# Optimization experiments

Hardware: AMD Instinct MI355X
Metric: run time of the kernel (lower is better)

## Reference

```python
import jax, jax.numpy as jnp
import numpy as np

B, T, D = 4, 2048, 1024
H, HD = 16, 64  # num_heads, head_size; H*HD == D
DFF = 4 * D
EPS = 1e-5

def _ln(x, g, b):
    mu = jnp.mean(x, axis=-1, keepdims=True)
    var = jnp.mean(jnp.square(x - mu), axis=-1, keepdims=True)
    return (x - mu) * jax.lax.rsqrt(var + EPS) * g + b

def setup_inputs() -> dict:
    key = jax.random.key(0)
    ks = jax.random.split(key, 12)
    s = lambda fan_in: 1.0 / np.sqrt(fan_in)
    return {
        "x": jax.random.normal(ks[0], (B, T, D), jnp.float32),
        "Wq": jax.random.normal(ks[1], (H, D, HD), jnp.float32) * s(D),
        "Wk": jax.random.normal(ks[2], (H, D, HD), jnp.float32) * s(D),
        "Wv": jax.random.normal(ks[3], (H, D, HD), jnp.float32) * s(D),
        "Wo": jax.random.normal(ks[4], (D, D), jnp.float32) * s(D),
        "bo": jax.random.normal(ks[5], (D,), jnp.float32) * 0.01,
        "W1": jax.random.normal(ks[6], (D, DFF), jnp.float32) * s(D),
        "b1": jax.random.normal(ks[7], (DFF,), jnp.float32) * 0.01,
        "W2": jax.random.normal(ks[8], (DFF, D), jnp.float32) * s(DFF),
        "b2": jax.random.normal(ks[9], (D,), jnp.float32) * 0.01,
        "g1": jnp.ones((D,), jnp.float32),
        "be1": jnp.zeros((D,), jnp.float32),
        "g2": jnp.ones((D,), jnp.float32),
        "be2": jnp.zeros((D,), jnp.float32),
    }

def reference(x, Wq, Wk, Wv, Wo, bo, W1, b1, W2, b2, g1, be1, g2, be2):
    # pre-LN attention
    h = _ln(x, g1, be1)                                   # [B,T,D]
    q = jnp.einsum('btd,hde->bhte', h, Wq)                # [B,H,T,HD]
    k = jnp.einsum('btd,hde->bhte', h, Wk)
    v = jnp.einsum('btd,hde->bhte', h, Wv)
    scores = jnp.einsum('bhte,bhse->bhts', q, k) * (HD ** -0.5)  # [B,H,T,T]
    mask = jnp.tril(jnp.ones((T, T), bool))
    scores = jnp.where(mask, scores, -jnp.inf)
    attn = jax.nn.softmax(scores, axis=-1)
    ctx = jnp.einsum('bhts,bhse->bhte', attn, v)          # [B,H,T,HD]
    ctx = ctx.transpose(0, 2, 1, 3).reshape(B, T, D)      # concat heads
    x = x + jnp.einsum('btd,de->bte', ctx, Wo) + bo
    # pre-LN FFN
    h2 = _ln(x, g2, be2)
    ff = jax.nn.relu(jnp.einsum('btd,df->btf', h2, W1) + b1)
    x = x + jnp.einsum('btf,fd->btd', ff, W2) + b2
    return x
```

## Files before the change

kernel.cpp:

```cpp
#include <hip/hip_runtime.h>
#include <stdint.h>

#define B_ 4
#define T_ 2048
#define D_ 1024
#define H_ 16
#define HD_ 64
#define DFF_ 4096
#define M_ (B_ * T_)

typedef __bf16 bf16x8 __attribute__((ext_vector_type(8)));
typedef float f32x4 __attribute__((ext_vector_type(4)));

__device__ __forceinline__ uint16_t f2bf(float f) {
  union { float f; uint32_t u; } v;
  v.f = f;
  uint32_t r = v.u + 0x7FFF + ((v.u >> 16) & 1);
  return (uint16_t)(r >> 16);
}

#define GLD_LDS(gp, lp)                                                        \
  __builtin_amdgcn_global_load_lds(                                            \
      (const __attribute__((address_space(1))) void*)(gp),                     \
      (__attribute__((address_space(3))) void*)(lp), 16, 0, 0)

__global__ __launch_bounds__(256) void ln_bf16(const float* __restrict__ x,
                                               const float* __restrict__ gamma,
                                               const float* __restrict__ beta,
                                               uint16_t* __restrict__ out) {
  __shared__ float red[4];
  const int tid = threadIdx.x;
  const size_t row = blockIdx.x;
  const float4 v = ((const float4*)(x + row * D_))[tid];
  float s = v.x + v.y + v.z + v.w;
#pragma unroll
  for (int off = 32; off >= 1; off >>= 1) s += __shfl_xor(s, off, 64);
  if ((tid & 63) == 0) red[tid >> 6] = s;
  __syncthreads();
  const float mean = (red[0] + red[1] + red[2] + red[3]) * (1.0f / D_);
  const float d0 = v.x - mean, d1 = v.y - mean, d2 = v.z - mean, d3 = v.w - mean;
  float ss = d0 * d0 + d1 * d1 + d2 * d2 + d3 * d3;
#pragma unroll
  for (int off = 32; off >= 1; off >>= 1) ss += __shfl_xor(ss, off, 64);
  __syncthreads();
  if ((tid & 63) == 0) red[tid >> 6] = ss;
  __syncthreads();
  const float var = (red[0] + red[1] + red[2] + red[3]) * (1.0f / D_);
  const float rstd = rsqrtf(var + 1e-5f);
  const float4 g = ((const float4*)gamma)[tid];
  const float4 b = ((const float4*)beta)[tid];
  ushort4 o;
  o.x = f2bf(d0 * rstd * g.x + b.x);
  o.y = f2bf(d1 * rstd * g.y + b.y);
  o.z = f2bf(d2 * rstd * g.z + b.z);
  o.w = f2bf(d3 * rstd * g.w + b.w);
  ((ushort4*)(out + row * D_))[tid] = o;
}

__global__ __launch_bounds__(256) void prep_ln(
    const float* __restrict__ x, const float* __restrict__ g1,
    const float* __restrict__ be1, uint16_t* __restrict__ hbuf,
    const float* __restrict__ Wq, const float* __restrict__ Wk,
    const float* __restrict__ Wv, const float* __restrict__ Wo,
    const float* __restrict__ W1, const float* __restrict__ W2,
    uint16_t* __restrict__ wqkvt, uint16_t* __restrict__ wot,
    uint16_t* __restrict__ w1t, uint16_t* __restrict__ w2t) {
  const int pid = blockIdx.x;
  const int tid = threadIdx.x;

  if (pid < 8192) {
    __shared__ float red[4];
    const size_t row = pid;
    const float4 v = ((const float4*)(x + row * D_))[tid];
    float s = v.x + v.y + v.z + v.w;
#pragma unroll
    for (int off = 32; off >= 1; off >>= 1) s += __shfl_xor(s, off, 64);
    if ((tid & 63) == 0) red[tid >> 6] = s;
    __syncthreads();
    const float mean = (red[0] + red[1] + red[2] + red[3]) * (1.0f / D_);
    const float d0 = v.x - mean, d1 = v.y - mean, d2 = v.z - mean, d3 = v.w - mean;
    float ss = d0 * d0 + d1 * d1 + d2 * d2 + d3 * d3;
#pragma unroll
    for (int off = 32; off >= 1; off >>= 1) ss += __shfl_xor(ss, off, 64);
    __syncthreads();
    if ((tid & 63) == 0) red[tid >> 6] = ss;
    __syncthreads();
    const float var = (red[0] + red[1] + red[2] + red[3]) * (1.0f / D_);
    const float rstd = rsqrtf(var + 1e-5f);
    const float4 g = ((const float4*)g1)[tid];
    const float4 b = ((const float4*)be1)[tid];
    ushort4 o;
    o.x = f2bf(d0 * rstd * g.x + b.x);
    o.y = f2bf(d1 * rstd * g.y + b.y);
    o.z = f2bf(d2 * rstd * g.z + b.z);
    o.w = f2bf(d3 * rstd * g.w + b.w);
    ((ushort4*)(hbuf + row * D_))[tid] = o;
    return;
  }

  __shared__ float tile[32][33];
  const int tx = tid & 31, ty = tid >> 5;
  const int q = pid - 8192;

  if (q >= 9216) {
    const int p = q - 9216;
    const int bx = p & 1, by = (p >> 1) & 31, z = p >> 6;
    const int which = z >> 4, hh = z & 15;
    const float* W = (which == 0) ? Wq : ((which == 1) ? Wk : Wv);
    const float* in = W + (size_t)hh * D_ * HD_;
    const int e0 = bx * 32, d0 = by * 32;
#pragma unroll
    for (int i = 0; i < 32; i += 8)
      tile[ty + i][tx] = in[(size_t)(d0 + ty + i) * HD_ + e0 + tx];
    __syncthreads();
#pragma unroll
    for (int i = 0; i < 32; i += 8)
      wqkvt[((size_t)(which * 1024 + hh * 64) + e0 + ty + i) * D_ + d0 + tx] =
          f2bf(tile[tx][ty + i]);
    return;
  }

  const float* in;
  uint16_t* out;
  int R, C, bx, by;
  if (q < 1024) {
    in = Wo; out = wot; R = 1024; C = 1024; bx = q & 31; by = q >> 5;
  } else if (q < 5120) {
    const int p = q - 1024;
    in = W1; out = w1t; R = 1024; C = 4096; bx = p & 127; by = p >> 7;
  } else {
    const int p = q - 5120;
    in = W2; out = w2t; R = 4096; C = 1024; bx = p & 31; by = p >> 5;
  }
  const int c0 = bx * 32, r0 = by * 32;
#pragma unroll
  for (int i = 0; i < 32; i += 8)
    tile[ty + i][tx] = in[(size_t)(r0 + ty + i) * C + c0 + tx];
  __syncthreads();
#pragma unroll
  for (int i = 0; i < 32; i += 8)
    out[(size_t)(c0 + ty + i) * R + r0 + tx] = f2bf(tile[tx][ty + i]);
}

template <int BN>
__global__ __launch_bounds__(256) void gemm_bf16(const uint16_t* __restrict__ A,
                                                 const uint16_t* __restrict__ Bt,
                                                 void* __restrict__ C,
                                                 const float* __restrict__ bias,
                                                 const float* __restrict__ resid,
                                                 int M, int N, int K, int lda,
                                                 int ldb, int flags) {
  constexpr int NJ = BN / 32;
  __shared__ __align__(16) uint16_t As[128 * 64];
  __shared__ __align__(16) uint16_t Bs[BN * 64];
  const int tid = threadIdx.x;
  const int lane = tid & 63, w = tid >> 6;
  const int quad = lane >> 4, lr = lane & 15;
  const int wr = w >> 1, wc = w & 1;

  const int n_tiles = N / BN;
  const int pid = blockIdx.x;
  const int grp = 16 * n_tiles;
  const int gid = pid / grp;
  const int rem = pid - gid * grp;
  const int nt = rem / 16;
  const int mt = gid * 16 + (rem - nt * 16);
  const int bn0 = nt * BN, bm0 = mt * 128;

  f32x4 acc[4][NJ];
#pragma unroll
  for (int i = 0; i < 4; i++)
#pragma unroll
    for (int j = 0; j < NJ; j++) acc[i][j] = f32x4{0.f, 0.f, 0.f, 0.f};

  const int s_row = lane >> 3, s_slot = lane & 7;

  for (int k0 = 0; k0 < K; k0 += 64) {
#pragma unroll
    for (int u = 0; u < 4; u++) {
      const int r = w * 32 + u * 8 + s_row;
      const int cg = s_slot ^ (r & 7);
      GLD_LDS(A + (size_t)(bm0 + r) * lda + k0 + cg * 8, As + (w * 32 + u * 8) * 64);
    }
#pragma unroll
    for (int u = 0; u < NJ; u++) {
      const int r = w * (BN / 4) + u * 8 + s_row;
      const int cg = s_slot ^ (r & 7);
      GLD_LDS(Bt + (size_t)(bn0 + r) * ldb + k0 + cg * 8,
              Bs + (w * (BN / 4) + u * 8) * 64);
    }
    __syncthreads();

#pragma unroll
    for (int ks = 0; ks < 2; ks++) {
      bf16x8 af[4], bfr[NJ];
#pragma unroll
      for (int i = 0; i < 4; i++) {
        const int m = wr * 64 + i * 16 + lr;
        const int slot = (ks * 4 + quad) ^ (m & 7);
        af[i] = *(const bf16x8*)(As + m * 64 + slot * 8);
      }
#pragma unroll
      for (int j = 0; j < NJ; j++) {
        const int n = wc * (BN / 2) + j * 16 + lr;
        const int slot = (ks * 4 + quad) ^ (n & 7);
        bfr[j] = *(const bf16x8*)(Bs + n * 64 + slot * 8);
      }
#pragma unroll
      for (int i = 0; i < 4; i++)
#pragma unroll
        for (int j = 0; j < NJ; j++)
          acc[i][j] =
              __builtin_amdgcn_mfma_f32_16x16x32_bf16(af[i], bfr[j], acc[i][j], 0, 0, 0);
    }
    __syncthreads();
  }

  const int base_m = bm0 + wr * 64 + quad * 4;
  const int base_n = bn0 + wc * (BN / 2) + lr;
#pragma unroll
  for (int i = 0; i < 4; i++) {
#pragma unroll
    for (int j = 0; j < NJ; j++) {
      const int col = base_n + j * 16;
      const float bv = bias ? bias[col] : 0.f;
#pragma unroll
      for (int r = 0; r < 4; r++) {
        const size_t row = base_m + i * 16 + r;
        float v = acc[i][j][r] + bv;
        if (resid) v += resid[row * N + col];
        if (flags & 1) v = fmaxf(v, 0.f);
        if (flags & 2)
          ((uint16_t*)C)[row * N + col] = f2bf(v);
        else
          ((float*)C)[row * N + col] = v;
      }
    }
  }
}

#define STAGE8(buf, kt)                                                        \
  do {                                                                         \
    const int k0s = (kt) * 64;                                                 \
    _Pragma("unroll") for (int u = 0; u < 4; u++) {                            \
      const int r = w * 32 + u * 8 + s_row;                                    \
      const int cg = s_slot ^ (r & 7);                                         \
      GLD_LDS(A + (size_t)(bm0 + r) * lda + k0s + cg * 8,                      \
              &As[buf][(w * 32 + u * 8) * 64]);                                \
      GLD_LDS(Bt + (size_t)(bn0 + r) * ldb + k0s + cg * 8,                     \
              &Bs[buf][(w * 32 + u * 8) * 64]);                                \
    }                                                                          \
  } while (0)

#define RD_A8(dst, ibase, ks)                                                  \
  _Pragma("unroll") for (int i = 0; i < 4; i++) {                              \
    const int m = wr * 128 + ((ibase) + i) * 16 + lr;                          \
    const int slot = ((ks) * 4 + quad) ^ (m & 7);                              \
    dst[i] = *(const bf16x8*)(&As[c][m * 64 + slot * 8]);                      \
  }

#define RD_B8(dst, ks)                                                         \
  _Pragma("unroll") for (int j = 0; j < 4; j++) {                              \
    const int n = wc * 64 + j * 16 + lr;                                       \
    const int slot = ((ks) * 4 + quad) ^ (n & 7);                              \
    dst[j] = *(const bf16x8*)(&Bs[c][n * 64 + slot * 8]);                      \
  }

#define MFMA16(ibase, aarr)                                                    \
  do {                                                                         \
    __builtin_amdgcn_s_setprio(1);                                             \
    _Pragma("unroll") for (int i = 0; i < 4; i++)                              \
        _Pragma("unroll") for (int j = 0; j < 4; j++) acc[(ibase) + i][j] =    \
        __builtin_amdgcn_mfma_f32_16x16x32_bf16(aarr[i], bb[j],                \
                                                acc[(ibase) + i][j], 0, 0, 0); \
    __builtin_amdgcn_s_setprio(0);                                             \
  } while (0)

__global__ __launch_bounds__(512, 2) void gemm_8ph(
    const uint16_t* __restrict__ A, const uint16_t* __restrict__ Bt,
    void* __restrict__ C, const float* __restrict__ bias,
    const float* __restrict__ resid, int M, int N, int K, int lda, int ldb,
    int flags) {
  __shared__ __align__(16) uint16_t As[2][256 * 64];
  __shared__ __align__(16) uint16_t Bs[2][256 * 64];
  const int tid = threadIdx.x;
  const int lane = tid & 63, w = tid >> 6;
  const int quad = lane >> 4, lr = lane & 15;
  const int wr = w >> 2, wc = w & 3;
  const int s_row = lane >> 3, s_slot = lane & 7;

  const int nwg = gridDim.x;
  const int cpx = nwg >> 3;
  const int pid0 = blockIdx.x;
  const int pid = (pid0 & 7) * cpx + (pid0 >> 3);
  const int n_tiles = N >> 8;
  const int mt = pid / n_tiles;
  const int nt = pid - mt * n_tiles;
  const int bm0 = mt * 256, bn0 = nt * 256;

  f32x4 acc[8][4];
#pragma unroll
  for (int i = 0; i < 8; i++)
#pragma unroll
    for (int j = 0; j < 4; j++) acc[i][j] = f32x4{0.f, 0.f, 0.f, 0.f};

  STAGE8(0, 0);
  asm volatile("s_waitcnt vmcnt(0)" ::: "memory");
  __builtin_amdgcn_s_barrier();

  const int NT = K >> 6;
  for (int t = 0; t < NT; ++t) {
    const int c = t & 1;
    bf16x8 a_lo[4], a_hi[4], bb[4];
    RD_A8(a_lo, 0, 0);
    RD_B8(bb, 0);
    if (t + 1 < NT) STAGE8(c ^ 1, t + 1);
    __builtin_amdgcn_s_barrier();
    MFMA16(0, a_lo);
    __builtin_amdgcn_s_barrier();
    RD_A8(a_hi, 4, 0);
    __builtin_amdgcn_s_barrier();
    MFMA16(4, a_hi);
    __builtin_amdgcn_s_barrier();
    RD_A8(a_lo, 0, 1);
    RD_B8(bb, 1);
    __builtin_amdgcn_s_barrier();
    MFMA16(0, a_lo);
    __builtin_amdgcn_s_barrier();
    RD_A8(a_hi, 4, 1);
    __builtin_amdgcn_s_barrier();
    MFMA16(4, a_hi);
    asm volatile("s_waitcnt vmcnt(0)" ::: "memory");
    __builtin_amdgcn_s_barrier();
  }

  const int base_m = bm0 + wr * 128 + quad * 4;
  const int base_n = bn0 + wc * 64 + lr;
#pragma unroll
  for (int i = 0; i < 8; i++) {
#pragma unroll
    for (int j = 0; j < 4; j++) {
      const int col = base_n + j * 16;
      const float bv = bias ? bias[col] : 0.f;
#pragma unroll
      for (int r = 0; r < 4; r++) {
        const size_t row = base_m + i * 16 + r;
        float v = acc[i][j][r] + bv;
        if (resid) v += resid[row * N + col];
        if (flags & 1) v = fmaxf(v, 0.f);
        if (flags & 2)
          ((uint16_t*)C)[row * N + col] = f2bf(v);
        else
          ((float*)C)[row * N + col] = v;
      }
    }
  }
}

__global__ __launch_bounds__(256) void v_transpose(const uint16_t* __restrict__ qkv,
                                                   uint16_t* __restrict__ vtb) {
  __shared__ __align__(16) uint16_t tile[64 * 72];
  const int tid = threadIdx.x;
  const int t0 = blockIdx.x * 64;
  const int bh = blockIdx.y;
  const int b = bh >> 4, h = bh & 15;
  const uint16_t* src = qkv + (size_t)b * T_ * 3072 + 2048 + h * 64;
#pragma unroll
  for (int u = 0; u < 2; u++) {
    const int uu = tid + u * 256;
    const int r = uu >> 3, c = uu & 7;
    *(int4*)(tile + r * 72 + c * 8) =
        *(const int4*)(src + (size_t)(t0 + r) * 3072 + c * 8);
  }
  __syncthreads();
  uint16_t* dst = vtb + ((size_t)bh * 64) * T_ + t0;
#pragma unroll
  for (int u = 0; u < 2; u++) {
    const int uu = tid + u * 256;
    const int e = uu >> 3, c2 = uu & 7;
    union { uint16_t u16[8]; int4 v; } tmp;
#pragma unroll
    for (int jj = 0; jj < 8; jj++) tmp.u16[jj] = tile[(c2 * 8 + jj) * 72 + e];
    *(int4*)(dst + (size_t)e * T_ + c2 * 8) = tmp.v;
  }
}

__device__ __forceinline__ void attn_tile_compute(
    const uint16_t* __restrict__ Kb, const uint16_t* __restrict__ Vb,
    uint16_t* __restrict__ Ps, const bf16x8 (&aq)[2][2], f32x4 (&oacc)[2][4],
    float (&l_part)[2], int st, int q0, int w, int quad, int lr) {
  const int lr7 = lr & 7;
  const int row_min_w = q0 + w * 32;

  f32x4 sa[2][4];
#pragma unroll
  for (int i = 0; i < 2; i++)
#pragma unroll
    for (int sf = 0; sf < 4; sf++) sa[i][sf] = f32x4{0.f, 0.f, 0.f, 0.f};
#pragma unroll
  for (int ks = 0; ks < 2; ks++) {
    bf16x8 ak[4];
#pragma unroll
    for (int sf = 0; sf < 4; sf++) {
      const int slot = (ks * 4 + quad) ^ lr7;
      ak[sf] = *(const bf16x8*)(Kb + (sf * 16 + lr) * 64 + slot * 8);
    }
#pragma unroll
    for (int i = 0; i < 2; i++)
#pragma unroll
      for (int sf = 0; sf < 4; sf++)
        sa[i][sf] =
            __builtin_amdgcn_mfma_f32_16x16x32_bf16(ak[sf], aq[i][ks], sa[i][sf], 0, 0, 0);
  }

  const bool diag = (st * 64 + 63 > row_min_w);
  if (diag) {
#pragma unroll
    for (int i = 0; i < 2; i++) {
      const int mrow = q0 + w * 32 + i * 16 + lr;
#pragma unroll
      for (int sf = 0; sf < 4; sf++) {
        const int s0 = st * 64 + sf * 16 + quad * 4;
        float p[4];
#pragma unroll
        for (int r = 0; r < 4; r++) {
          float sv = sa[i][sf][r];
          if (s0 + r > mrow) sv = -1e30f;
          p[r] = exp2f(fmaf(sv, 0.18033688f, -28.8539008f));
          l_part[i] += p[r];
        }
        ushort4 pk;
        pk.x = f2bf(p[0]);
        pk.y = f2bf(p[1]);
        pk.z = f2bf(p[2]);
        pk.w = f2bf(p[3]);
        *(ushort4*)(Ps + (size_t)(w * 32 + i * 16 + lr) * 72 + sf * 16 + quad * 4) = pk;
      }
    }
  } else {
#pragma unroll
    for (int i = 0; i < 2; i++) {
#pragma unroll
      for (int sf = 0; sf < 4; sf++) {
        float p[4];
#pragma unroll
        for (int r = 0; r < 4; r++) {
          p[r] = exp2f(fmaf(sa[i][sf][r], 0.18033688f, -28.8539008f));
          l_part[i] += p[r];
        }
        ushort4 pk;
        pk.x = f2bf(p[0]);
        pk.y = f2bf(p[1]);
        pk.z = f2bf(p[2]);
        pk.w = f2bf(p[3]);
        *(ushort4*)(Ps + (size_t)(w * 32 + i * 16 + lr) * 72 + sf * 16 + quad * 4) = pk;
      }
    }
  }

#pragma unroll
  for (int ks = 0; ks < 2; ks++) {
    bf16x8 ap[2], bv[4];
#pragma unroll
    for (int i = 0; i < 2; i++)
      ap[i] = *(const bf16x8*)(Ps + (size_t)(w * 32 + i * 16 + lr) * 72 + ks * 32 +
                               quad * 8);
#pragma unroll
    for (int j = 0; j < 4; j++) {
      const int slot = (ks * 4 + quad) ^ lr7;
      bv[j] = *(const bf16x8*)(Vb + (j * 16 + lr) * 64 + slot * 8);
    }
#pragma unroll
    for (int i = 0; i < 2; i++)
#pragma unroll
      for (int j = 0; j < 4; j++)
        oacc[i][j] =
            __builtin_amdgcn_mfma_f32_16x16x32_bf16(ap[i], bv[j], oacc[i][j], 0, 0, 0);
  }
}

__global__ __launch_bounds__(256) void attn_mfma(const uint16_t* __restrict__ qkv,
                                                 const uint16_t* __restrict__ vtb,
                                                 uint16_t* __restrict__ ctx) {
  __shared__ __align__(16) uint16_t Ks[64 * 64];
  __shared__ __align__(16) uint16_t Vt[64 * 64];
  __shared__ __align__(16) uint16_t Ps[128 * 72];
  const int tid = threadIdx.x;
  const int lane = tid & 63, w = tid >> 6;
  const int quad = lane >> 4, lr = lane & 15;
  const int pid = blockIdx.x;
  const int bh = pid & 63;
  const int i_pair = pid >> 6;
  const int b = bh >> 4, h = bh & 15;
  const uint16_t* base = qkv + (size_t)b * T_ * 3072 + h * 64;
  const uint16_t* vbase = vtb + ((size_t)bh * 64) * T_;
  const int s_row = lane >> 3, s_slot = lane & 7;

  const int tqA = i_pair, tqB = 15 - i_pair;
  const int q0A = tqA * 128, q0B = tqB * 128;
  const int nstgA = 2 * tqA + 2, nstgB = 2 * tqB + 2;
  const int nstg = (nstgA > nstgB) ? nstgA : nstgB;

  bf16x8 aqA[2][2], aqB[2][2];
#pragma unroll
  for (int i = 0; i < 2; i++)
#pragma unroll
    for (int ks = 0; ks < 2; ks++) {
      aqA[i][ks] = *(const bf16x8*)(base + (size_t)(q0A + w * 32 + i * 16 + lr) * 3072 +
                                    ks * 32 + quad * 8);
      aqB[i][ks] = *(const bf16x8*)(base + (size_t)(q0B + w * 32 + i * 16 + lr) * 3072 +
                                    ks * 32 + quad * 8);
    }

  f32x4 oaccA[2][4], oaccB[2][4];
#pragma unroll
  for (int i = 0; i < 2; i++)
#pragma unroll
    for (int j = 0; j < 4; j++) {
      oaccA[i][j] = f32x4{0.f, 0.f, 0.f, 0.f};
      oaccB[i][j] = f32x4{0.f, 0.f, 0.f, 0.f};
    }
  float lA[2] = {0.f, 0.f}, lB[2] = {0.f, 0.f};

  const int row_maxA = q0A + w * 32 + 31;
  const int row_maxB = q0B + w * 32 + 31;

  for (int st = 0; st < nstg; st++) {
    __syncthreads();
#pragma unroll
    for (int u = 0; u < 2; u++) {
      const int r = w * 16 + u * 8 + s_row;
      const int cg = s_slot ^ (r & 7);
      GLD_LDS(base + 1024 + (size_t)(st * 64 + r) * 3072 + cg * 8,
              Ks + (w * 16 + u * 8) * 64);
      GLD_LDS(vbase + (size_t)r * T_ + st * 64 + cg * 8, Vt + (w * 16 + u * 8) * 64);
    }
    __syncthreads();

    if (st < nstgA && st * 64 <= row_maxA)
      attn_tile_compute(Ks, Vt, Ps, aqA, oaccA, lA, st, q0A, w, quad, lr);
    if (st < nstgB && st * 64 <= row_maxB)
      attn_tile_compute(Ks, Vt, Ps, aqB, oaccB, lB, st, q0B, w, quad, lr);
  }

#pragma unroll
  for (int half = 0; half < 2; half++) {
    const int q0 = half ? q0B : q0A;
    f32x4(&oacc)[2][4] = half ? oaccB : oaccA;
    float* l_part = half ? lB : lA;
    float linv[2];
#pragma unroll
    for (int i = 0; i < 2; i++) {
      float l = l_part[i];
      l += __shfl_xor(l, 16, 64);
      l += __shfl_xor(l, 32, 64);
      linv[i] = 1.f / l;
    }
    uint16_t* ob =
        ctx + ((size_t)b * T_ + q0 + w * 32 + quad * 4) * D_ + h * 64 + lr;
#pragma unroll
    for (int i = 0; i < 2; i++)
#pragma unroll
      for (int r = 0; r < 4; r++) {
        const float inv = __shfl(linv[i], quad * 4 + r, 64);
#pragma unroll
        for (int j = 0; j < 4; j++)
          ob[(size_t)(i * 16 + r) * D_ + j * 16] = f2bf(oacc[i][j][r] * inv);
      }
  }
}

extern "C" void kernel_launch(void* const* d_in, const int* in_sizes, int n_in,
                              void* d_out, int out_size, void* d_ws, size_t ws_size,
                              hipStream_t stream) {
  const float* x = (const float*)d_in[0];
  const float* Wq = (const float*)d_in[1];
  const float* Wk = (const float*)d_in[2];
  const float* Wv = (const float*)d_in[3];
  const float* Wo = (const float*)d_in[4];
  const float* bo = (const float*)d_in[5];
  const float* W1 = (const float*)d_in[6];
  const float* b1 = (const float*)d_in[7];
  const float* W2 = (const float*)d_in[8];
  const float* b2 = (const float*)d_in[9];
  const float* g1 = (const float*)d_in[10];
  const float* be1 = (const float*)d_in[11];
  const float* g2 = (const float*)d_in[12];
  const float* be2 = (const float*)d_in[13];
  float* out = (float*)d_out;

  const size_t MB = 1024ull * 1024ull;
  if (ws_size < 200 * MB) return;
  char* ws = (char*)d_ws;
  uint16_t* hbuf = (uint16_t*)(ws + 0 * MB);
  uint16_t* wqkvt = (uint16_t*)(ws + 16 * MB);
  uint16_t* wot = (uint16_t*)(ws + 22 * MB);
  uint16_t* w1t = (uint16_t*)(ws + 24 * MB);
  uint16_t* w2t = (uint16_t*)(ws + 32 * MB);
  float* x1 = (float*)(ws + 40 * MB);
  uint16_t* qkvb = (uint16_t*)(ws + 72 * MB);
  uint16_t* ctxb = (uint16_t*)(ws + 120 * MB);
  uint16_t* vtb = (uint16_t*)(ws + 136 * MB);
  uint16_t* ffb = (uint16_t*)(ws + 136 * MB);

  prep_ln<<<20480, 256, 0, stream>>>(x, g1, be1, hbuf, Wq, Wk, Wv, Wo, W1, W2,
                                     wqkvt, wot, w1t, w2t);
  gemm_8ph<<<(M_ / 256) * (3 * D_ / 256), 512, 0, stream>>>(
      hbuf, wqkvt, qkvb, nullptr, nullptr, M_, 3 * D_, D_, D_, D_, 2);
  v_transpose<<<dim3(T_ / 64, B_ * H_), 256, 0, stream>>>(qkvb, vtb);
  attn_mfma<<<512, 256, 0, stream>>>(qkvb, vtb, ctxb);
  gemm_bf16<64><<<64 * 16, 256, 0, stream>>>(ctxb, wot, x1, bo, x, M_, D_, D_, D_,
                                             D_, 0);
  ln_bf16<<<M_, 256, 0, stream>>>(x1, g2, be2, hbuf);
  gemm_8ph<<<(M_ / 256) * (DFF_ / 256), 512, 0, stream>>>(
      hbuf, w1t, ffb, b1, nullptr, M_, DFF_, D_, D_, D_, 1 | 2);
  gemm_bf16<64><<<64 * 16, 256, 0, stream>>>(ffb, w2t, out, b2, x1, M_, D_, DFF_,
                                             DFF_, DFF_, 0);
}
```

Baseline: 559.9 us.

## Split A-tile staging by half and use partial vmcnt waits in GEMM pipeline

Reorders the global-to-LDS staging so each wave loads A rows grouped by the upper and lower 128-row halves. Partial s_waitcnt vmcnt counts then let the first half of A be consumed before the second half of the prefetch has landed. The last K iteration is peeled so the steady-state loop always prefetches, and the peeled tail drops its intra-iteration barriers. The aim is to overlap the prefetch with MFMA work instead of draining all loads at the end of each iteration. The risk is that the vmcnt counts depend on exact load issue order, so any mismatch would mean reading stale LDS data.

```diff
diff --git a/kernel.cpp b/kernel.cpp
--- a/kernel.cpp
+++ b/kernel.cpp
@@ -245,10 +245,21 @@
     _Pragma("unroll") for (int u = 0; u < 4; u++) {                            \
       const int r = w * 32 + u * 8 + s_row;                                    \
       const int cg = s_slot ^ (r & 7);                                         \
-      GLD_LDS(A + (size_t)(bm0 + r) * lda + k0s + cg * 8,                      \
-              &As[buf][(w * 32 + u * 8) * 64]);                                \
       GLD_LDS(Bt + (size_t)(bn0 + r) * ldb + k0s + cg * 8,                     \
               &Bs[buf][(w * 32 + u * 8) * 64]);                                \
+    }                                                                          \
+    const int rb = (w >> 2) * 128 + (w & 3) * 16;                              \
+    _Pragma("unroll") for (int u = 0; u < 2; u++) {                            \
+      const int r = rb + u * 8 + s_row;                                        \
+      const int cg = s_slot ^ (r & 7);                                         \
+      GLD_LDS(A + (size_t)(bm0 + r) * lda + k0s + cg * 8,                      \
+              &As[buf][(rb + u * 8) * 64]);                                    \
+    }                                                                          \
+    _Pragma("unroll") for (int u = 0; u < 2; u++) {                            \
+      const int r = rb + 64 + u * 8 + s_row;                                   \
+      const int cg = s_slot ^ (r & 7);                                         \
+      GLD_LDS(A + (size_t)(bm0 + r) * lda + k0s + cg * 8,                      \
+              &As[buf][(rb + 64 + u * 8) * 64]);                               \
     }                                                                          \
   } while (0)
 
@@ -275,6 +286,8 @@
                                                 acc[(ibase) + i][j], 0, 0, 0); \
     __builtin_amdgcn_s_setprio(0);                                             \
   } while (0)
+
+#define VMW(n) asm volatile("s_waitcnt vmcnt(" #n ")" ::: "memory")
 
 __global__ __launch_bounds__(512, 2) void gemm_8ph(
     const uint16_t* __restrict__ A, const uint16_t* __restrict__ Bt,
@@ -305,33 +318,51 @@
     for (int j = 0; j < 4; j++) acc[i][j] = f32x4{0.f, 0.f, 0.f, 0.f};
 
   STAGE8(0, 0);
-  asm volatile("s_waitcnt vmcnt(0)" ::: "memory");
+  VMW(2);
   __builtin_amdgcn_s_barrier();
 
   const int NT = K >> 6;
-  for (int t = 0; t < NT; ++t) {
+  for (int t = 0; t < NT - 1; ++t) {
     const int c = t & 1;
+    bf16x8 a_lo[4], a_hi[4], bb[4];
+    STAGE8(c ^ 1, t + 1);
+    RD_A8(a_lo, 0, 0);
+    RD_B8(bb, 0);
+    __builtin_amdgcn_s_barrier();
+    MFMA16(0, a_lo);
+    VMW(8);
+    __builtin_amdgcn_s_barrier();
+    RD_A8(a_hi, 4, 0);
+    __builtin_amdgcn_s_barrier();
+    MFMA16(4, a_hi);
+    __builtin_amdgcn_s_barrier();
+    RD_A8(a_lo, 0, 1);
+    RD_B8(bb, 1);
+    __builtin_amdgcn_s_barrier();
+    MFMA16(0, a_lo);
+    __builtin_amdgcn_s_barrier();
+    RD_A8(a_hi, 4, 1);
+    __builtin_amdgcn_s_barrier();
+    MFMA16(4, a_hi);
+    VMW(2);
+    __builtin_amdgcn_s_barrier();
+  }
+  {
+    const int c = (NT - 1) & 1;
     bf16x8 a_lo[4], a_hi[4], bb[4];
     RD_A8(a_lo, 0, 0);
     RD_B8(bb, 0);
-    if (t + 1 < NT) STAGE8(c ^ 1, t + 1);
     __builtin_amdgcn_s_barrier();
     MFMA16(0, a_lo);
+    VMW(0);
     __builtin_amdgcn_s_barrier();
     RD_A8(a_hi, 4, 0);
-    __builtin_amdgcn_s_barrier();
     MFMA16(4, a_hi);
-    __builtin_amdgcn_s_barrier();
     RD_A8(a_lo, 0, 1);
     RD_B8(bb, 1);
-    __builtin_amdgcn_s_barrier();
     MFMA16(0, a_lo);
-    __builtin_amdgcn_s_barrier();
     RD_A8(a_hi, 4, 1);
-    __builtin_amdgcn_s_barrier();
     MFMA16(4, a_hi);
-    asm volatile("s_waitcnt vmcnt(0)" ::: "memory");
-    __builtin_amdgcn_s_barrier();
   }
 
   const int base_m = bm0 + wr * 128 + quad * 4;
```

Result: faster. 548.1 us (-2.1%).

## Interleave gemm_8ph global-to-LDS staging across phases and switch QKV GEMM kernel

Applied to the files above, without the earlier changes.

Rewrites the 8-phase GEMM main loop so the next K-tile's global-to-LDS loads are split into four quarter-stages spread across the MFMA phases, with partial vmcnt waits instead of a full drain each tile. The loop is unrolled by two tiles and ends in an explicit epilogue. The aim is to hide global memory latency behind MFMA work without stalling at every tile boundary. Separately, the QKV projection now uses gemm_bf16<128> instead of gemm_8ph, so the rewritten pipeline only runs in the FFN W1 GEMM. The wait counts must match the number of outstanding loads, and the loop assumes K is a multiple of 128.

```diff
diff --git a/kernel.cpp b/kernel.cpp
--- a/kernel.cpp
+++ b/kernel.cpp
@@ -239,31 +239,39 @@
   }
 }
 
-#define STAGE8(buf, kt)                                                        \
+#define STAGE_PAIR(buf, kt, p)                                                 \
   do {                                                                         \
     const int k0s = (kt) * 64;                                                 \
-    _Pragma("unroll") for (int u = 0; u < 4; u++) {                            \
-      const int r = w * 32 + u * 8 + s_row;                                    \
-      const int cg = s_slot ^ (r & 7);                                         \
-      GLD_LDS(A + (size_t)(bm0 + r) * lda + k0s + cg * 8,                      \
-              &As[buf][(w * 32 + u * 8) * 64]);                                \
-      GLD_LDS(Bt + (size_t)(bn0 + r) * ldb + k0s + cg * 8,                     \
-              &Bs[buf][(w * 32 + u * 8) * 64]);                                \
+    if ((p) < 2) {                                                             \
+      _Pragma("unroll") for (int u = 0; u < 2; u++) {                          \
+        const int r = w * 32 + ((p) * 2 + u) * 8 + s_row;                      \
+        const int cg = s_slot ^ (r & 7);                                       \
+        GLD_LDS(Bt + (size_t)(bn0 + r) * ldb + k0s + cg * 8,                   \
+                &Bs[buf][(w * 32 + ((p) * 2 + u) * 8) * 64]);                  \
+      }                                                                        \
+    } else {                                                                   \
+      const int rb = (w >> 2) * 128 + (w & 3) * 16 + ((p) - 2) * 64;           \
+      _Pragma("unroll") for (int u = 0; u < 2; u++) {                          \
+        const int r = rb + u * 8 + s_row;                                      \
+        const int cg = s_slot ^ (r & 7);                                       \
+        GLD_LDS(A + (size_t)(bm0 + r) * lda + k0s + cg * 8,                    \
+                &As[buf][(rb + u * 8) * 64]);                                  \
+      }                                                                        \
     }                                                                          \
   } while (0)
 
-#define RD_A8(dst, ibase, ks)                                                  \
+#define RD_A8Q(dst, ibase, ks, BUF)                                            \
   _Pragma("unroll") for (int i = 0; i < 4; i++) {                              \
     const int m = wr * 128 + ((ibase) + i) * 16 + lr;                          \
     const int slot = ((ks) * 4 + quad) ^ (m & 7);                              \
-    dst[i] = *(const bf16x8*)(&As[c][m * 64 + slot * 8]);                      \
-  }
-
-#define RD_B8(dst, ks)                                                         \
+    dst[i] = *(const bf16x8*)(&As[BUF][m * 64 + slot * 8]);                    \
+  }
+
+#define RD_B8Q(dst, ks, BUF)                                                   \
   _Pragma("unroll") for (int j = 0; j < 4; j++) {                              \
     const int n = wc * 64 + j * 16 + lr;                                       \
     const int slot = ((ks) * 4 + quad) ^ (n & 7);                              \
-    dst[j] = *(const bf16x8*)(&Bs[c][n * 64 + slot * 8]);                      \
+    dst[j] = *(const bf16x8*)(&Bs[BUF][n * 64 + slot * 8]);                    \
   }
 
 #define MFMA16(ibase, aarr)                                                    \
@@ -275,6 +283,9 @@
                                                 acc[(ibase) + i][j], 0, 0, 0); \
     __builtin_amdgcn_s_setprio(0);                                             \
   } while (0)
+
+#define VMW(n) asm volatile("s_waitcnt vmcnt(" #n ")" ::: "memory")
+#define BAR() __builtin_amdgcn_s_barrier()
 
 __global__ __launch_bounds__(512, 2) void gemm_8ph(
     const uint16_t* __restrict__ A, const uint16_t* __restrict__ Bt,
@@ -304,34 +315,106 @@
 #pragma unroll
     for (int j = 0; j < 4; j++) acc[i][j] = f32x4{0.f, 0.f, 0.f, 0.f};
 
-  STAGE8(0, 0);
-  asm volatile("s_waitcnt vmcnt(0)" ::: "memory");
-  __builtin_amdgcn_s_barrier();
-
-  const int NT = K >> 6;
-  for (int t = 0; t < NT; ++t) {
-    const int c = t & 1;
-    bf16x8 a_lo[4], a_hi[4], bb[4];
-    RD_A8(a_lo, 0, 0);
-    RD_B8(bb, 0);
-    if (t + 1 < NT) STAGE8(c ^ 1, t + 1);
-    __builtin_amdgcn_s_barrier();
-    MFMA16(0, a_lo);
-    __builtin_amdgcn_s_barrier();
-    RD_A8(a_hi, 4, 0);
-    __builtin_amdgcn_s_barrier();
-    MFMA16(4, a_hi);
-    __builtin_amdgcn_s_barrier();
-    RD_A8(a_lo, 0, 1);
-    RD_B8(bb, 1);
-    __builtin_amdgcn_s_barrier();
-    MFMA16(0, a_lo);
-    __builtin_amdgcn_s_barrier();
-    RD_A8(a_hi, 4, 1);
-    __builtin_amdgcn_s_barrier();
-    MFMA16(4, a_hi);
-    asm volatile("s_waitcnt vmcnt(0)" ::: "memory");
-    __builtin_amdgcn_s_barrier();
+  STAGE_PAIR(0, 0, 0);
+  STAGE_PAIR(0, 0, 1);
+  STAGE_PAIR(0, 0, 2);
+  STAGE_PAIR(0, 0, 3);
+  STAGE_PAIR(1, 1, 0);
+  VMW(2);
+  BAR();
+
+  const int NIT = K >> 7;
+  for (int it = 0; it < NIT - 1; ++it) {
+    const int v = 2 * it + 1, wt = 2 * it + 2, vn = 2 * it + 3;
+    bf16x8 a0[4], a1[4], bb[4];
+    RD_A8Q(a0, 0, 0, 0);
+    RD_B8Q(bb, 0, 0);
+    STAGE_PAIR(1, v, 1);
+    BAR();
+    MFMA16(0, a0);
+    BAR();
+    RD_A8Q(a1, 4, 0, 0);
+    STAGE_PAIR(1, v, 2);
+    BAR();
+    MFMA16(4, a1);
+    BAR();
+    RD_A8Q(a0, 0, 1, 0);
+    RD_B8Q(bb, 1, 0);
+    STAGE_PAIR(1, v, 3);
+    BAR();
+    MFMA16(0, a0);
+    BAR();
+    RD_A8Q(a1, 4, 1, 0);
+    STAGE_PAIR(0, wt, 0);
+    BAR();
+    MFMA16(4, a1);
+    VMW(2);
+    BAR();
+    RD_A8Q(a0, 0, 0, 1);
+    RD_B8Q(bb, 0, 1);
+    STAGE_PAIR(0, wt, 1);
+    BAR();
+    MFMA16(0, a0);
+    BAR();
+    RD_A8Q(a1, 4, 0, 1);
+    STAGE_PAIR(0, wt, 2);
+    BAR();
+    MFMA16(4, a1);
+    BAR();
+    RD_A8Q(a0, 0, 1, 1);
+    RD_B8Q(bb, 1, 1);
+    STAGE_PAIR(0, wt, 3);
+    BAR();
+    MFMA16(0, a0);
+    BAR();
+    RD_A8Q(a1, 4, 1, 1);
+    STAGE_PAIR(1, vn, 0);
+    BAR();
+    MFMA16(4, a1);
+    VMW(2);
+    BAR();
+  }
+  {
+    const int vL = (K >> 6) - 1;
+    bf16x8 a0[4], a1[4], bb[4];
+    RD_A8Q(a0, 0, 0, 0);
+    RD_B8Q(bb, 0, 0);
+    STAGE_PAIR(1, vL, 1);
+    BAR();
+    MFMA16(0, a0);
+    BAR();
+    RD_A8Q(a1, 4, 0, 0);
+    STAGE_PAIR(1, vL, 2);
+    BAR();
+    MFMA16(4, a1);
+    BAR();
+    RD_A8Q(a0, 0, 1, 0);
+    RD_B8Q(bb, 1, 0);
+    STAGE_PAIR(1, vL, 3);
+    BAR();
+    MFMA16(0, a0);
+    BAR();
+    RD_A8Q(a1, 4, 1, 0);
+    BAR();
+    MFMA16(4, a1);
+    VMW(0);
+    BAR();
+    RD_A8Q(a0, 0, 0, 1);
+    RD_B8Q(bb, 0, 1);
+    BAR();
+    MFMA16(0, a0);
+    BAR();
+    RD_A8Q(a1, 4, 0, 1);
+    BAR();
+    MFMA16(4, a1);
+    BAR();
+    RD_A8Q(a0, 0, 1, 1);
+    RD_B8Q(bb, 1, 1);
+    BAR();
+    MFMA16(0, a0);
+    BAR();
+    RD_A8Q(a1, 4, 1, 1);
+    MFMA16(4, a1);
   }
 
   const int base_m = bm0 + wr * 128 + quad * 4;
@@ -605,8 +688,8 @@
 
   prep_ln<<<20480, 256, 0, stream>>>(x, g1, be1, hbuf, Wq, Wk, Wv, Wo, W1, W2,
                                      wqkvt, wot, w1t, w2t);
-  gemm_8ph<<<(M_ / 256) * (3 * D_ / 256), 512, 0, stream>>>(
-      hbuf, wqkvt, qkvb, nullptr, nullptr, M_, 3 * D_, D_, D_, D_, 2);
+  gemm_bf16<128><<<64 * 24, 256, 0, stream>>>(hbuf, wqkvt, qkvb, nullptr, nullptr,
+                                              M_, 3 * D_, D_, D_, D_, 2);
   v_transpose<<<dim3(T_ / 64, B_ * H_), 256, 0, stream>>>(qkvb, vtb);
   attn_mfma<<<512, 256, 0, stream>>>(qkvb, vtb, ctxb);
   gemm_bf16<64><<<64 * 16, 256, 0, stream>>>(ctxb, wot, x1, bo, x, M_, D_, D_, D_,
```

Result: faster. 521.9 us (-6.8%).
